# Kernel optimization log

Hardware: AMD Instinct MI355X
Metric: run time of the kernel (lower is better)

## Reference

```python
import jax, jax.numpy as jnp
import numpy as np

E, TOPK, H, I = 8, 2, 2048, 5632
T = 4096


def setup_inputs() -> dict:
    key = jax.random.key(0)
    k1, k2, k3, k4 = jax.random.split(key, 4)
    hidden_states = jax.random.normal(k1, (T, H), dtype=jnp.float32)
    gate_w = jax.random.normal(k2, (E, H), dtype=jnp.float32) * (1.0 / np.sqrt(H))
    # fused gate+up projection: [E, 2*I, H]
    w13 = jax.random.normal(k3, (E, 2 * I, H), dtype=jnp.float32) * (1.0 / np.sqrt(H))
    # down projection: [E, H, I]
    w2 = jax.random.normal(k4, (E, H, I), dtype=jnp.float32) * (1.0 / np.sqrt(I))
    return {"hidden_states": hidden_states, "gate_w": gate_w, "w13": w13, "w2": w2, "top_k": TOPK}


def reference(hidden_states, gate_w, w13, w2, top_k):
    num_experts = gate_w.shape[0]
    inter = w2.shape[2]
    # router: fp32 gate logits -> softmax -> top-k -> renormalize (FusedMoE renormalize=True)
    logits = hidden_states.astype(jnp.float32) @ gate_w.T          # [T, E]
    probs = jax.nn.softmax(logits, axis=-1)
    vals, idx = jax.lax.top_k(probs, top_k)                        # [T, k]
    vals = vals / jnp.sum(vals, axis=-1, keepdims=True)
    # dense routing weight matrix [T, E] (zero outside top-k)
    dense_w = jnp.sum(jax.nn.one_hot(idx, num_experts, dtype=vals.dtype) * vals[..., None], axis=1)

    def body(acc, inputs):
        w13_e, w2_e, we = inputs                                   # [2I,H], [H,I], [T]
        gu = hidden_states @ w13_e.T                               # [T, 2I]
        g, u = gu[:, :inter], gu[:, inter:]
        h = jax.nn.silu(g) * u                                     # SwiGLU
        y = h @ w2_e.T                                             # [T, H]
        return acc + we[:, None] * y, None

    acc0 = jnp.zeros_like(hidden_states)
    out, _ = jax.lax.scan(body, acc0, (w13, w2, dense_w.T))
    return out
```

## Files before the change

### kernel.cpp

```cpp
#include <hip/hip_runtime.h>

#define T_TOK 4096
#define H_DIM 2048
#define I_DIM 5632
#define NE 8

typedef _Float16 f16;
typedef _Float16 f16x8 __attribute__((ext_vector_type(8)));
typedef _Float16 f16x4 __attribute__((ext_vector_type(4)));
typedef float f32x4 __attribute__((ext_vector_type(4)));

#define OFF_META   0
#define OFF_BTOK   256
#define OFF_BW     (256 + 32768)
#define OFF_RE     (256 + 2 * 32768)
#define OFF_RW     (256 + 3 * 32768)
#define OFF_HSB    (256 + 4 * 32768)
#define OFF_HB     (OFF_HSB + (size_t)T_TOK * H_DIM * 2)

__device__ __forceinline__ int swz(int row, int bir) {
    return (bir & 15) | ((((bir >> 4) ^ row) & 3) << 4);
}

__global__ void cvt_hs_kernel(const float* __restrict__ hs, f16* __restrict__ hsb) {
    size_t i = ((size_t)blockIdx.x * 256 + threadIdx.x) * 8;
    float4 a = *(const float4*)(hs + i);
    float4 b = *(const float4*)(hs + i + 4);
    f16x8 v;
    v[0] = (f16)a.x; v[1] = (f16)a.y; v[2] = (f16)a.z; v[3] = (f16)a.w;
    v[4] = (f16)b.x; v[5] = (f16)b.y; v[6] = (f16)b.z; v[7] = (f16)b.w;
    *(f16x8*)(hsb + i) = v;
}

__global__ void gate_kernel(const float* __restrict__ hs, const float* __restrict__ gw,
                            int* __restrict__ re, float* __restrict__ rw,
                            int* __restrict__ counts) {
    int lane = threadIdx.x & 63;
    int t = blockIdx.x * 4 + (threadIdx.x >> 6);
    float acc[NE];
#pragma unroll
    for (int e = 0; e < NE; ++e) acc[e] = 0.f;
    const float* x = hs + (size_t)t * H_DIM;
    for (int i = lane; i < H_DIM; i += 64) {
        float xv = x[i];
#pragma unroll
        for (int e = 0; e < NE; ++e) acc[e] += xv * gw[e * H_DIM + i];
    }
#pragma unroll
    for (int e = 0; e < NE; ++e)
        for (int off = 32; off > 0; off >>= 1) acc[e] += __shfl_xor(acc[e], off);
    if (lane == 0) {
        int i1 = 0; float l1 = acc[0];
#pragma unroll
        for (int e = 1; e < NE; ++e) if (acc[e] > l1) { l1 = acc[e]; i1 = e; }
        int i2 = -1; float l2 = -1e30f;
#pragma unroll
        for (int e = 0; e < NE; ++e) if (e != i1 && acc[e] > l2) { l2 = acc[e]; i2 = e; }
        float aa = __expf(l2 - l1);
        float s = 1.f / (1.f + aa);
        re[t * 2] = i1; re[t * 2 + 1] = i2;
        rw[t * 2] = s;  rw[t * 2 + 1] = aa * s;
        atomicAdd(&counts[i1], 1);
        atomicAdd(&counts[i2], 1);
    }
}

__global__ void scan_kernel(int* __restrict__ meta) {
    if (threadIdx.x == 0) {
        int s = 0;
        for (int e = 0; e < NE; ++e) { meta[8 + e] = s; meta[16 + e] = s; s += meta[e]; }
    }
}

__global__ void place_kernel(const int* __restrict__ re, const float* __restrict__ rw,
                             int* __restrict__ cursor, int* __restrict__ btok,
                             float* __restrict__ bwv) {
    int t = blockIdx.x * 256 + threadIdx.x;
    if (t >= T_TOK) return;
#pragma unroll
    for (int s = 0; s < 2; ++s) {
        int e = re[t * 2 + s];
        int p = atomicAdd(&cursor[e], 1);
        btok[p] = t;
        bwv[p] = rw[t * 2 + s];
    }
}

__global__ __launch_bounds__(256) void gemm1_kernel(
    const float* __restrict__ w13, const f16* __restrict__ hsb, f16* __restrict__ hb,
    const int* __restrict__ counts, const int* __restrict__ offs,
    const int* __restrict__ btok, int e_arg, int global_h)
{
    const int e = (e_arg >= 0) ? e_arg : (int)blockIdx.z;
    const int n_e = counts[e];
    const int by = blockIdx.y;
    if (by * 128 >= n_e) return;
    const int boff = offs[e];
    const int bx = blockIdx.x;
    const float* We = w13 + (size_t)e * (2 * I_DIM) * H_DIM;

    const int tid = threadIdx.x;
    const int lane = tid & 63;
    const int wid = tid >> 6;
    const int wm = wid >> 1, wn = wid & 1;

    __shared__ f16 As[128 * 32];
    __shared__ f16 Bgs[64 * 32];
    __shared__ f16 Bus[64 * 32];
    char* AsB = (char*)As; char* BgB = (char*)Bgs; char* BuB = (char*)Bus;

    const f16* gA[2];
#pragma unroll
    for (int i = 0; i < 2; ++i) {
        int c = i * 256 + tid;
        int r = c >> 2;
        int idx = by * 128 + r;
        idx = idx < n_e ? idx : (n_e - 1);
        int tok = btok[boff + idx];
        gA[i] = hsb + (size_t)tok * H_DIM + (c & 3) * 8;
    }
    const float* gBg[2]; const float* gBu[2];
#pragma unroll
    for (int j = 0; j < 2; ++j) {
        int lin = j * 256 + tid;
        int r = lin >> 3;
        int k = (lin & 7) * 4;
        gBg[j] = We + (size_t)(bx * 64 + r) * H_DIM + k;
        gBu[j] = We + (size_t)(I_DIM + bx * 64 + r) * H_DIM + k;
    }

    f32x4 accg[4][2], accu[4][2];
#pragma unroll
    for (int m = 0; m < 4; ++m)
#pragma unroll
        for (int n = 0; n < 2; ++n) { accg[m][n] = (f32x4)0.f; accu[m][n] = (f32x4)0.f; }

    const int NT = H_DIM / 32;
    f16x8 av0, av1; float4 bg0, bg1, bu0, bu1;
    av0 = *(const f16x8*)(gA[0]); av1 = *(const f16x8*)(gA[1]);
    bg0 = *(const float4*)(gBg[0]); bg1 = *(const float4*)(gBg[1]);
    bu0 = *(const float4*)(gBu[0]); bu1 = *(const float4*)(gBu[1]);

    for (int kt = 0; kt < NT; ++kt) {
        __syncthreads();
        {
            int c = tid;               int r = c >> 2;
            *(f16x8*)(AsB + r * 64 + swz(r, (c & 3) * 16)) = av0;
            c = 256 + tid;             r = c >> 2;
            *(f16x8*)(AsB + r * 64 + swz(r, (c & 3) * 16)) = av1;
        }
#pragma unroll
        for (int j = 0; j < 2; ++j) {
            int lin = j * 256 + tid; int r = lin >> 3; int bir = (lin & 7) * 8;
            float4 bg = j ? bg1 : bg0;
            float4 bu = j ? bu1 : bu0;
            f16x4 g4, u4;
            g4[0] = (f16)bg.x; g4[1] = (f16)bg.y; g4[2] = (f16)bg.z; g4[3] = (f16)bg.w;
            u4[0] = (f16)bu.x; u4[1] = (f16)bu.y; u4[2] = (f16)bu.z; u4[3] = (f16)bu.w;
            *(f16x4*)(BgB + r * 64 + swz(r, bir)) = g4;
            *(f16x4*)(BuB + r * 64 + swz(r, bir)) = u4;
        }
        __syncthreads();
        if (kt + 1 < NT) {
            int k0 = (kt + 1) * 32;
            av0 = *(const f16x8*)(gA[0] + k0); av1 = *(const f16x8*)(gA[1] + k0);
            bg0 = *(const float4*)(gBg[0] + k0); bg1 = *(const float4*)(gBg[1] + k0);
            bu0 = *(const float4*)(gBu[0] + k0); bu1 = *(const float4*)(gBu[1] + k0);
        }
        f16x8 a[4], bgf[2], buf_[2];
        const int kb = (lane >> 4) * 16;
#pragma unroll
        for (int m = 0; m < 4; ++m) {
            int r = wm * 64 + m * 16 + (lane & 15);
            a[m] = *(const f16x8*)(AsB + r * 64 + swz(r, kb));
        }
#pragma unroll
        for (int n = 0; n < 2; ++n) {
            int r = wn * 32 + n * 16 + (lane & 15);
            bgf[n]  = *(const f16x8*)(BgB + r * 64 + swz(r, kb));
            buf_[n] = *(const f16x8*)(BuB + r * 64 + swz(r, kb));
        }
#pragma unroll
        for (int m = 0; m < 4; ++m)
#pragma unroll
            for (int n = 0; n < 2; ++n) {
                accg[m][n] = __builtin_amdgcn_mfma_f32_16x16x32_f16(a[m], bgf[n],  accg[m][n], 0, 0, 0);
                accu[m][n] = __builtin_amdgcn_mfma_f32_16x16x32_f16(a[m], buf_[n], accu[m][n], 0, 0, 0);
            }
    }
    const int hbase = (global_h ? boff : 0) + by * 128;
#pragma unroll
    for (int m = 0; m < 4; ++m) {
        int rl0 = wm * 64 + m * 16 + ((lane >> 4) << 2);
#pragma unroll
        for (int r = 0; r < 4; ++r) {
            int rl = rl0 + r;
            if (by * 128 + rl < n_e) {
#pragma unroll
                for (int n = 0; n < 2; ++n) {
                    float g = accg[m][n][r];
                    float u = accu[m][n][r];
                    float h = g / (1.f + __expf(-g)) * u;
                    hb[(size_t)(hbase + rl) * I_DIM + bx * 64 + wn * 32 + n * 16 + (lane & 15)] = (f16)h;
                }
            }
        }
    }
}

__global__ __launch_bounds__(256) void gemm2_kernel(
    const float* __restrict__ w2, const f16* __restrict__ hb, float* __restrict__ out,
    const int* __restrict__ counts, const int* __restrict__ offs,
    const int* __restrict__ btok, const float* __restrict__ bwv, int e_arg, int global_h)
{
    const int e = (e_arg >= 0) ? e_arg : (int)blockIdx.z;
    const int n_e = counts[e];
    const int by = blockIdx.y;
    if (by * 128 >= n_e) return;
    const int boff = offs[e];
    const int bx = blockIdx.x;
    const float* We = w2 + (size_t)e * H_DIM * I_DIM;

    const int tid = threadIdx.x;
    const int lane = tid & 63;
    const int wid = tid >> 6;
    const int wm = wid >> 1, wn = wid & 1;

    __shared__ f16 As[128 * 32];
    __shared__ f16 Bs[128 * 32];
    char* AsB = (char*)As; char* BsB = (char*)Bs;

    const int hbase = (global_h ? boff : 0) + by * 128;
    const f16* gA[2];
#pragma unroll
    for (int i = 0; i < 2; ++i) {
        int c = i * 256 + tid;
        int r = c >> 2;
        gA[i] = hb + (size_t)(hbase + r) * I_DIM + (c & 3) * 8;
    }
    const float* gB[4];
#pragma unroll
    for (int j = 0; j < 4; ++j) {
        int lin = j * 256 + tid;
        int r = lin >> 3;
        int k = (lin & 7) * 4;
        gB[j] = We + (size_t)(bx * 128 + r) * I_DIM + k;
    }

    f32x4 acc[4][4];
#pragma unroll
    for (int m = 0; m < 4; ++m)
#pragma unroll
        for (int n = 0; n < 4; ++n) acc[m][n] = (f32x4)0.f;

    const int NT = I_DIM / 32;
    f16x8 av0, av1; float4 bv0, bv1, bv2, bv3;
    av0 = *(const f16x8*)(gA[0]); av1 = *(const f16x8*)(gA[1]);
    bv0 = *(const float4*)(gB[0]); bv1 = *(const float4*)(gB[1]);
    bv2 = *(const float4*)(gB[2]); bv3 = *(const float4*)(gB[3]);

    for (int kt = 0; kt < NT; ++kt) {
        __syncthreads();
        {
            int c = tid;       int r = c >> 2;
            *(f16x8*)(AsB + r * 64 + swz(r, (c & 3) * 16)) = av0;
            c = 256 + tid;     r = c >> 2;
            *(f16x8*)(AsB + r * 64 + swz(r, (c & 3) * 16)) = av1;
        }
#pragma unroll
        for (int j = 0; j < 4; ++j) {
            int lin = j * 256 + tid; int r = lin >> 3; int bir = (lin & 7) * 8;
            float4 b = (j == 0) ? bv0 : (j == 1) ? bv1 : (j == 2) ? bv2 : bv3;
            f16x4 b4;
            b4[0] = (f16)b.x; b4[1] = (f16)b.y; b4[2] = (f16)b.z; b4[3] = (f16)b.w;
            *(f16x4*)(BsB + r * 64 + swz(r, bir)) = b4;
        }
        __syncthreads();
        if (kt + 1 < NT) {
            int k0 = (kt + 1) * 32;
            av0 = *(const f16x8*)(gA[0] + k0); av1 = *(const f16x8*)(gA[1] + k0);
            bv0 = *(const float4*)(gB[0] + k0); bv1 = *(const float4*)(gB[1] + k0);
            bv2 = *(const float4*)(gB[2] + k0); bv3 = *(const float4*)(gB[3] + k0);
        }
        f16x8 a[4], b[4];
        const int kb = (lane >> 4) * 16;
#pragma unroll
        for (int m = 0; m < 4; ++m) {
            int r = wm * 64 + m * 16 + (lane & 15);
            a[m] = *(const f16x8*)(AsB + r * 64 + swz(r, kb));
        }
#pragma unroll
        for (int n = 0; n < 4; ++n) {
            int r = wn * 64 + n * 16 + (lane & 15);
            b[n] = *(const f16x8*)(BsB + r * 64 + swz(r, kb));
        }
#pragma unroll
        for (int m = 0; m < 4; ++m)
#pragma unroll
            for (int n = 0; n < 4; ++n)
                acc[m][n] = __builtin_amdgcn_mfma_f32_16x16x32_f16(a[m], b[n], acc[m][n], 0, 0, 0);
    }
#pragma unroll
    for (int m = 0; m < 4; ++m) {
        int rl0 = wm * 64 + m * 16 + ((lane >> 4) << 2);
#pragma unroll
        for (int r = 0; r < 4; ++r) {
            int rl = rl0 + r;
            if (by * 128 + rl < n_e) {
                int p = boff + by * 128 + rl;
                int tok = btok[p];
                float w = bwv[p];
#pragma unroll
                for (int n = 0; n < 4; ++n) {
                    atomicAdd(&out[(size_t)tok * H_DIM + bx * 128 + wn * 64 + n * 16 + (lane & 15)],
                              w * acc[m][n][r]);
                }
            }
        }
    }
}

extern "C" void kernel_launch(void* const* d_in, const int* in_sizes, int n_in,
                              void* d_out, int out_size, void* d_ws, size_t ws_size,
                              hipStream_t stream) {
    const float* hs  = (const float*)d_in[0];
    const float* gw  = (const float*)d_in[1];
    const float* w13 = (const float*)d_in[2];
    const float* w2  = (const float*)d_in[3];
    float* out = (float*)d_out;

    char* ws = (char*)d_ws;
    int*   meta = (int*)(ws + OFF_META);
    int*   btok = (int*)(ws + OFF_BTOK);
    float* bwv  = (float*)(ws + OFF_BW);
    int*   re   = (int*)(ws + OFF_RE);
    float* rw   = (float*)(ws + OFF_RW);
    f16*   hsb  = (f16*)(ws + OFF_HSB);
    f16*   hb   = (f16*)(ws + OFF_HB);

    hipMemsetAsync(d_out, 0, (size_t)T_TOK * H_DIM * 4, stream);
    hipMemsetAsync(meta, 0, 256, stream);

    cvt_hs_kernel<<<(T_TOK * H_DIM) / (256 * 8), 256, 0, stream>>>(hs, hsb);
    gate_kernel<<<T_TOK / 4, 256, 0, stream>>>(hs, gw, re, rw, meta);
    scan_kernel<<<1, 64, 0, stream>>>(meta);
    place_kernel<<<T_TOK / 256, 256, 0, stream>>>(re, rw, meta + 16, btok, bwv);

    size_t need_allpairs = OFF_HB + (size_t)(2 * T_TOK + 128) * I_DIM * 2;
    if (ws_size >= need_allpairs) {
        gemm1_kernel<<<dim3(I_DIM / 64, T_TOK / 128, NE), 256, 0, stream>>>(
            w13, hsb, hb, meta, meta + 8, btok, -1, 1);
        gemm2_kernel<<<dim3(H_DIM / 128, T_TOK / 128, NE), 256, 0, stream>>>(
            w2, hb, out, meta, meta + 8, btok, bwv, -1, 1);
    } else {
        for (int e = 0; e < NE; ++e) {
            gemm1_kernel<<<dim3(I_DIM / 64, T_TOK / 128, 1), 256, 0, stream>>>(
                w13, hsb, hb, meta, meta + 8, btok, e, 0);
            gemm2_kernel<<<dim3(H_DIM / 128, T_TOK / 128, 1), 256, 0, stream>>>(
                w2, hb, out, meta, meta + 8, btok, bwv, e, 0);
        }
    }
}
```

Measured before the change: 1.405 ms.

## Double-buffer MoE GEMMs with direct global-to-LDS loads, larger tiles, XCD-aware block remap

Both expert GEMMs move to 512-thread blocks with 256-row M tiles and 64-wide K steps. LDS is now double-buffered: activation tiles are loaded with global_load_lds, and weight tiles are converted to fp16 and written into the next buffer while MFMAs run on the current one, synchronised by manual waitcnt and barriers. The grid is flattened to 1D with a remap that spreads logical tiles across the 8 XCDs for better L2 locality. This aims to overlap memory with compute and halve barrier count, at the cost of more LDS per block and fragile hand-written wait counts.

```diff
diff --git a/kernel.cpp b/kernel.cpp
--- a/kernel.cpp
+++ b/kernel.cpp
@@ -18,8 +18,19 @@
 #define OFF_HSB    (256 + 4 * 32768)
 #define OFF_HB     (OFF_HSB + (size_t)T_TOK * H_DIM * 2)
 
-__device__ __forceinline__ int swz(int row, int bir) {
-    return (bir & 15) | ((((bir >> 4) ^ row) & 3) << 4);
+typedef const __attribute__((address_space(1))) unsigned int guint;
+typedef __attribute__((address_space(3))) unsigned int luint;
+
+#define WAITVM4()  asm volatile("s_waitcnt vmcnt(4)" ::: "memory")
+#define WAITVM0()  asm volatile("s_waitcnt vmcnt(0)" ::: "memory")
+#define WAITLG0()  asm volatile("s_waitcnt lgkmcnt(0)" ::: "memory")
+
+__device__ __forceinline__ int swzk(int r, int bir) {
+    return (bir & 15) | ((((bir >> 4) ^ r) & 7) << 4);
+}
+
+__device__ __forceinline__ f16x4 cvt4(float4 v) {
+    f16x4 t; t[0] = (f16)v.x; t[1] = (f16)v.y; t[2] = (f16)v.z; t[3] = (f16)v.w; return t;
 }
 
 __global__ void cvt_hs_kernel(const float* __restrict__ hs, f16* __restrict__ hsb) {
@@ -86,17 +97,24 @@
     }
 }
 
-__global__ __launch_bounds__(256) void gemm1_kernel(
+__global__ __launch_bounds__(512, 2) void gemm1_kernel(
     const float* __restrict__ w13, const f16* __restrict__ hsb, f16* __restrict__ hb,
     const int* __restrict__ counts, const int* __restrict__ offs,
     const int* __restrict__ btok, int e_arg, int global_h)
 {
-    const int e = (e_arg >= 0) ? e_arg : (int)blockIdx.z;
+    const int nwg = gridDim.x;
+    const int cpx = nwg >> 3;
+    const int lin = blockIdx.x;
+    const int logical = (lin & 7) * cpx + (lin >> 3);
+    const int by = logical & 15;
+    const int rest = logical >> 4;
+    int bx, e;
+    if (e_arg >= 0) { bx = rest; e = e_arg; }
+    else            { bx = rest % 88; e = rest / 88; }
+
     const int n_e = counts[e];
-    const int by = blockIdx.y;
-    if (by * 128 >= n_e) return;
+    if (by * 256 >= n_e) return;
     const int boff = offs[e];
-    const int bx = blockIdx.x;
     const float* We = w13 + (size_t)e * (2 * I_DIM) * H_DIM;
 
     const int tid = threadIdx.x;
@@ -104,29 +122,36 @@
     const int wid = tid >> 6;
     const int wm = wid >> 1, wn = wid & 1;
 
-    __shared__ f16 As[128 * 32];
-    __shared__ f16 Bgs[64 * 32];
-    __shared__ f16 Bus[64 * 32];
-    char* AsB = (char*)As; char* BgB = (char*)Bgs; char* BuB = (char*)Bus;
-
-    const f16* gA[2];
-#pragma unroll
-    for (int i = 0; i < 2; ++i) {
-        int c = i * 256 + tid;
-        int r = c >> 2;
-        int idx = by * 128 + r;
-        idx = idx < n_e ? idx : (n_e - 1);
+    __shared__ f16 As[2][256 * 64];
+    __shared__ f16 Bg[2][64 * 64];
+    __shared__ f16 Bu[2][64 * 64];
+    char* AsB = (char*)As;
+    char* BgB = (char*)Bg;
+    char* BuB = (char*)Bu;
+
+    const f16* gA[4];
+    int cgrp[4];
+#pragma unroll
+    for (int i = 0; i < 4; ++i) {
+        int c = wid * 4 + i;
+        cgrp[i] = c;
+        int r = c * 8 + (lane >> 3);
+        int idx = by * 256 + r;
+        idx = idx < n_e ? idx : n_e - 1;
         int tok = btok[boff + idx];
-        gA[i] = hsb + (size_t)tok * H_DIM + (c & 3) * 8;
+        int sg = (lane & 7) ^ (lane >> 3);
+        gA[i] = hsb + (size_t)tok * H_DIM + sg * 8;
     }
     const float* gBg[2]; const float* gBu[2];
+    int bwadr[2];
 #pragma unroll
     for (int j = 0; j < 2; ++j) {
-        int lin = j * 256 + tid;
-        int r = lin >> 3;
-        int k = (lin & 7) * 4;
-        gBg[j] = We + (size_t)(bx * 64 + r) * H_DIM + k;
-        gBu[j] = We + (size_t)(I_DIM + bx * 64 + r) * H_DIM + k;
+        int c = j * 512 + tid;
+        int r = c >> 4;
+        int k4 = c & 15;
+        gBg[j] = We + (size_t)(bx * 64 + r) * H_DIM + k4 * 4;
+        gBu[j] = We + (size_t)(I_DIM + bx * 64 + r) * H_DIM + k4 * 4;
+        bwadr[j] = r * 128 + swzk(r, k4 * 8);
     }
 
     f32x4 accg[4][2], accu[4][2];
@@ -135,67 +160,85 @@
 #pragma unroll
         for (int n = 0; n < 2; ++n) { accg[m][n] = (f32x4)0.f; accu[m][n] = (f32x4)0.f; }
 
-    const int NT = H_DIM / 32;
-    f16x8 av0, av1; float4 bg0, bg1, bu0, bu1;
-    av0 = *(const f16x8*)(gA[0]); av1 = *(const f16x8*)(gA[1]);
-    bg0 = *(const float4*)(gBg[0]); bg1 = *(const float4*)(gBg[1]);
-    bu0 = *(const float4*)(gBu[0]); bu1 = *(const float4*)(gBu[1]);
-
+    const int NT = H_DIM / 64;
+
+    {
+        float4 g0 = *(const float4*)gBg[0];
+        float4 g1 = *(const float4*)gBg[1];
+        float4 u0 = *(const float4*)gBu[0];
+        float4 u1 = *(const float4*)gBu[1];
+        *(f16x4*)(BgB + bwadr[0]) = cvt4(g0);
+        *(f16x4*)(BgB + bwadr[1]) = cvt4(g1);
+        *(f16x4*)(BuB + bwadr[0]) = cvt4(u0);
+        *(f16x4*)(BuB + bwadr[1]) = cvt4(u1);
+#pragma unroll
+        for (int i = 0; i < 4; ++i)
+            __builtin_amdgcn_global_load_lds((guint*)(gA[i]), (luint*)(AsB + cgrp[i] * 1024), 16, 0, 0);
+    }
+
+    int cur = 0;
+#pragma unroll 1
     for (int kt = 0; kt < NT; ++kt) {
-        __syncthreads();
+        const int ktn = (kt + 1 < NT) ? kt + 1 : NT - 1;
+        float4 g0 = *(const float4*)(gBg[0] + ktn * 64);
+        float4 g1 = *(const float4*)(gBg[1] + ktn * 64);
+        float4 u0 = *(const float4*)(gBu[0] + ktn * 64);
+        float4 u1 = *(const float4*)(gBu[1] + ktn * 64);
+        WAITVM4();
+        WAITLG0();
+        __builtin_amdgcn_s_barrier();
+        __builtin_amdgcn_sched_barrier(0);
+#pragma unroll
+        for (int i = 0; i < 4; ++i)
+            __builtin_amdgcn_global_load_lds((guint*)(gA[i] + ktn * 64),
+                (luint*)(AsB + (cur ^ 1) * 32768 + cgrp[i] * 1024), 16, 0, 0);
+        const char* Ab = AsB + cur * 32768;
+        const char* Gb = BgB + cur * 8192;
+        const char* Ub = BuB + cur * 8192;
+#pragma unroll
+        for (int kh = 0; kh < 2; ++kh) {
+            f16x8 a[4], bg[2], bu[2];
+            const int kb = kh * 64 + (lane >> 4) * 16;
+#pragma unroll
+            for (int m = 0; m < 4; ++m) {
+                int r = wm * 64 + m * 16 + (lane & 15);
+                a[m] = *(const f16x8*)(Ab + r * 128 + swzk(r, kb));
+            }
+#pragma unroll
+            for (int n = 0; n < 2; ++n) {
+                int r = wn * 32 + n * 16 + (lane & 15);
+                bg[n] = *(const f16x8*)(Gb + r * 128 + swzk(r, kb));
+                bu[n] = *(const f16x8*)(Ub + r * 128 + swzk(r, kb));
+            }
+#pragma unroll
+            for (int m = 0; m < 4; ++m)
+#pragma unroll
+                for (int n = 0; n < 2; ++n) {
+                    accg[m][n] = __builtin_amdgcn_mfma_f32_16x16x32_f16(a[m], bg[n], accg[m][n], 0, 0, 0);
+                    accu[m][n] = __builtin_amdgcn_mfma_f32_16x16x32_f16(a[m], bu[n], accu[m][n], 0, 0, 0);
+                }
+        }
+        WAITVM4();
         {
-            int c = tid;               int r = c >> 2;
-            *(f16x8*)(AsB + r * 64 + swz(r, (c & 3) * 16)) = av0;
-            c = 256 + tid;             r = c >> 2;
-            *(f16x8*)(AsB + r * 64 + swz(r, (c & 3) * 16)) = av1;
-        }
-#pragma unroll
-        for (int j = 0; j < 2; ++j) {
-            int lin = j * 256 + tid; int r = lin >> 3; int bir = (lin & 7) * 8;
-            float4 bg = j ? bg1 : bg0;
-            float4 bu = j ? bu1 : bu0;
-            f16x4 g4, u4;
-            g4[0] = (f16)bg.x; g4[1] = (f16)bg.y; g4[2] = (f16)bg.z; g4[3] = (f16)bg.w;
-            u4[0] = (f16)bu.x; u4[1] = (f16)bu.y; u4[2] = (f16)bu.z; u4[3] = (f16)bu.w;
-            *(f16x4*)(BgB + r * 64 + swz(r, bir)) = g4;
-            *(f16x4*)(BuB + r * 64 + swz(r, bir)) = u4;
-        }
-        __syncthreads();
-        if (kt + 1 < NT) {
-            int k0 = (kt + 1) * 32;
-            av0 = *(const f16x8*)(gA[0] + k0); av1 = *(const f16x8*)(gA[1] + k0);
-            bg0 = *(const float4*)(gBg[0] + k0); bg1 = *(const float4*)(gBg[1] + k0);
-            bu0 = *(const float4*)(gBu[0] + k0); bu1 = *(const float4*)(gBu[1] + k0);
-        }
-        f16x8 a[4], bgf[2], buf_[2];
-        const int kb = (lane >> 4) * 16;
-#pragma unroll
-        for (int m = 0; m < 4; ++m) {
-            int r = wm * 64 + m * 16 + (lane & 15);
-            a[m] = *(const f16x8*)(AsB + r * 64 + swz(r, kb));
-        }
-#pragma unroll
-        for (int n = 0; n < 2; ++n) {
-            int r = wn * 32 + n * 16 + (lane & 15);
-            bgf[n]  = *(const f16x8*)(BgB + r * 64 + swz(r, kb));
-            buf_[n] = *(const f16x8*)(BuB + r * 64 + swz(r, kb));
-        }
-#pragma unroll
-        for (int m = 0; m < 4; ++m)
-#pragma unroll
-            for (int n = 0; n < 2; ++n) {
-                accg[m][n] = __builtin_amdgcn_mfma_f32_16x16x32_f16(a[m], bgf[n],  accg[m][n], 0, 0, 0);
-                accu[m][n] = __builtin_amdgcn_mfma_f32_16x16x32_f16(a[m], buf_[n], accu[m][n], 0, 0, 0);
-            }
-    }
-    const int hbase = (global_h ? boff : 0) + by * 128;
+            char* Gn = BgB + (cur ^ 1) * 8192;
+            char* Un = BuB + (cur ^ 1) * 8192;
+            *(f16x4*)(Gn + bwadr[0]) = cvt4(g0);
+            *(f16x4*)(Gn + bwadr[1]) = cvt4(g1);
+            *(f16x4*)(Un + bwadr[0]) = cvt4(u0);
+            *(f16x4*)(Un + bwadr[1]) = cvt4(u1);
+        }
+        cur ^= 1;
+    }
+    WAITVM0();
+
+    const int hbase = (global_h ? boff : 0) + by * 256;
 #pragma unroll
     for (int m = 0; m < 4; ++m) {
         int rl0 = wm * 64 + m * 16 + ((lane >> 4) << 2);
 #pragma unroll
         for (int r = 0; r < 4; ++r) {
             int rl = rl0 + r;
-            if (by * 128 + rl < n_e) {
+            if (by * 256 + rl < n_e) {
 #pragma unroll
                 for (int n = 0; n < 2; ++n) {
                     float g = accg[m][n][r];
@@ -208,17 +251,24 @@
     }
 }
 
-__global__ __launch_bounds__(256) void gemm2_kernel(
+__global__ __launch_bounds__(512, 2) void gemm2_kernel(
     const float* __restrict__ w2, const f16* __restrict__ hb, float* __restrict__ out,
     const int* __restrict__ counts, const int* __restrict__ offs,
     const int* __restrict__ btok, const float* __restrict__ bwv, int e_arg, int global_h)
 {
-    const int e = (e_arg >= 0) ? e_arg : (int)blockIdx.z;
+    const int nwg = gridDim.x;
+    const int cpx = nwg >> 3;
+    const int lin = blockIdx.x;
+    const int logical = (lin & 7) * cpx + (lin >> 3);
+    const int by = logical & 15;
+    const int rest = logical >> 4;
+    int bx, e;
+    if (e_arg >= 0) { bx = rest; e = e_arg; }
+    else            { bx = rest % 16; e = rest / 16; }
+
     const int n_e = counts[e];
-    const int by = blockIdx.y;
-    if (by * 128 >= n_e) return;
+    if (by * 256 >= n_e) return;
     const int boff = offs[e];
-    const int bx = blockIdx.x;
     const float* We = w2 + (size_t)e * H_DIM * I_DIM;
 
     const int tid = threadIdx.x;
@@ -226,25 +276,31 @@
     const int wid = tid >> 6;
     const int wm = wid >> 1, wn = wid & 1;
 
-    __shared__ f16 As[128 * 32];
-    __shared__ f16 Bs[128 * 32];
-    char* AsB = (char*)As; char* BsB = (char*)Bs;
-
-    const int hbase = (global_h ? boff : 0) + by * 128;
-    const f16* gA[2];
-#pragma unroll
-    for (int i = 0; i < 2; ++i) {
-        int c = i * 256 + tid;
-        int r = c >> 2;
-        gA[i] = hb + (size_t)(hbase + r) * I_DIM + (c & 3) * 8;
+    __shared__ f16 As[2][256 * 64];
+    __shared__ f16 Bs[2][128 * 64];
+    char* AsB = (char*)As;
+    char* BsB = (char*)Bs;
+
+    const int hbase = (global_h ? boff : 0) + by * 256;
+    const f16* gA[4];
+    int cgrp[4];
+#pragma unroll
+    for (int i = 0; i < 4; ++i) {
+        int c = wid * 4 + i;
+        cgrp[i] = c;
+        int r = c * 8 + (lane >> 3);
+        int sg = (lane & 7) ^ (lane >> 3);
+        gA[i] = hb + (size_t)(hbase + r) * I_DIM + sg * 8;
     }
     const float* gB[4];
+    int bwadr[4];
 #pragma unroll
     for (int j = 0; j < 4; ++j) {
-        int lin = j * 256 + tid;
-        int r = lin >> 3;
-        int k = (lin & 7) * 4;
-        gB[j] = We + (size_t)(bx * 128 + r) * I_DIM + k;
+        int c = j * 512 + tid;
+        int r = c >> 4;
+        int k4 = c & 15;
+        gB[j] = We + (size_t)(bx * 128 + r) * I_DIM + k4 * 4;
+        bwadr[j] = r * 128 + swzk(r, k4 * 8);
     }
 
     f32x4 acc[4][4];
@@ -253,68 +309,86 @@
 #pragma unroll
         for (int n = 0; n < 4; ++n) acc[m][n] = (f32x4)0.f;
 
-    const int NT = I_DIM / 32;
-    f16x8 av0, av1; float4 bv0, bv1, bv2, bv3;
-    av0 = *(const f16x8*)(gA[0]); av1 = *(const f16x8*)(gA[1]);
-    bv0 = *(const float4*)(gB[0]); bv1 = *(const float4*)(gB[1]);
-    bv2 = *(const float4*)(gB[2]); bv3 = *(const float4*)(gB[3]);
-
+    const int NT = I_DIM / 64;
+
+    {
+        float4 b0 = *(const float4*)gB[0];
+        float4 b1 = *(const float4*)gB[1];
+        float4 b2 = *(const float4*)gB[2];
+        float4 b3 = *(const float4*)gB[3];
+        *(f16x4*)(BsB + bwadr[0]) = cvt4(b0);
+        *(f16x4*)(BsB + bwadr[1]) = cvt4(b1);
+        *(f16x4*)(BsB + bwadr[2]) = cvt4(b2);
+        *(f16x4*)(BsB + bwadr[3]) = cvt4(b3);
+#pragma unroll
+        for (int i = 0; i < 4; ++i)
+            __builtin_amdgcn_global_load_lds((guint*)(gA[i]), (luint*)(AsB + cgrp[i] * 1024), 16, 0, 0);
+    }
+
+    int cur = 0;
+#pragma unroll 1
     for (int kt = 0; kt < NT; ++kt) {
-        __syncthreads();
+        const int ktn = (kt + 1 < NT) ? kt + 1 : NT - 1;
+        float4 b0 = *(const float4*)(gB[0] + ktn * 64);
+        float4 b1 = *(const float4*)(gB[1] + ktn * 64);
+        float4 b2 = *(const float4*)(gB[2] + ktn * 64);
+        float4 b3 = *(const float4*)(gB[3] + ktn * 64);
+        WAITVM4();
+        WAITLG0();
+        __builtin_amdgcn_s_barrier();
+        __builtin_amdgcn_sched_barrier(0);
+#pragma unroll
+        for (int i = 0; i < 4; ++i)
+            __builtin_amdgcn_global_load_lds((guint*)(gA[i] + ktn * 64),
+                (luint*)(AsB + (cur ^ 1) * 32768 + cgrp[i] * 1024), 16, 0, 0);
+        const char* Ab = AsB + cur * 32768;
+        const char* Bb = BsB + cur * 16384;
+#pragma unroll
+        for (int kh = 0; kh < 2; ++kh) {
+            f16x8 a[4], b[4];
+            const int kb = kh * 64 + (lane >> 4) * 16;
+#pragma unroll
+            for (int m = 0; m < 4; ++m) {
+                int r = wm * 64 + m * 16 + (lane & 15);
+                a[m] = *(const f16x8*)(Ab + r * 128 + swzk(r, kb));
+            }
+#pragma unroll
+            for (int n = 0; n < 4; ++n) {
+                int r = wn * 64 + n * 16 + (lane & 15);
+                b[n] = *(const f16x8*)(Bb + r * 128 + swzk(r, kb));
+            }
+#pragma unroll
+            for (int m = 0; m < 4; ++m)
+#pragma unroll
+                for (int n = 0; n < 4; ++n)
+                    acc[m][n] = __builtin_amdgcn_mfma_f32_16x16x32_f16(a[m], b[n], acc[m][n], 0, 0, 0);
+        }
+        WAITVM4();
         {
-            int c = tid;       int r = c >> 2;
-            *(f16x8*)(AsB + r * 64 + swz(r, (c & 3) * 16)) = av0;
-            c = 256 + tid;     r = c >> 2;
-            *(f16x8*)(AsB + r * 64 + swz(r, (c & 3) * 16)) = av1;
-        }
-#pragma unroll
-        for (int j = 0; j < 4; ++j) {
-            int lin = j * 256 + tid; int r = lin >> 3; int bir = (lin & 7) * 8;
-            float4 b = (j == 0) ? bv0 : (j == 1) ? bv1 : (j == 2) ? bv2 : bv3;
-            f16x4 b4;
-            b4[0] = (f16)b.x; b4[1] = (f16)b.y; b4[2] = (f16)b.z; b4[3] = (f16)b.w;
-            *(f16x4*)(BsB + r * 64 + swz(r, bir)) = b4;
-        }
-        __syncthreads();
-        if (kt + 1 < NT) {
-            int k0 = (kt + 1) * 32;
-            av0 = *(const f16x8*)(gA[0] + k0); av1 = *(const f16x8*)(gA[1] + k0);
-            bv0 = *(const float4*)(gB[0] + k0); bv1 = *(const float4*)(gB[1] + k0);
-            bv2 = *(const float4*)(gB[2] + k0); bv3 = *(const float4*)(gB[3] + k0);
-        }
-        f16x8 a[4], b[4];
-        const int kb = (lane >> 4) * 16;
-#pragma unroll
-        for (int m = 0; m < 4; ++m) {
-            int r = wm * 64 + m * 16 + (lane & 15);
-            a[m] = *(const f16x8*)(AsB + r * 64 + swz(r, kb));
-        }
-#pragma unroll
-        for (int n = 0; n < 4; ++n) {
-            int r = wn * 64 + n * 16 + (lane & 15);
-            b[n] = *(const f16x8*)(BsB + r * 64 + swz(r, kb));
-        }
-#pragma unroll
-        for (int m = 0; m < 4; ++m)
-#pragma unroll
-            for (int n = 0; n < 4; ++n)
-                acc[m][n] = __builtin_amdgcn_mfma_f32_16x16x32_f16(a[m], b[n], acc[m][n], 0, 0, 0);
-    }
+            char* Bn = BsB + (cur ^ 1) * 16384;
+            *(f16x4*)(Bn + bwadr[0]) = cvt4(b0);
+            *(f16x4*)(Bn + bwadr[1]) = cvt4(b1);
+            *(f16x4*)(Bn + bwadr[2]) = cvt4(b2);
+            *(f16x4*)(Bn + bwadr[3]) = cvt4(b3);
+        }
+        cur ^= 1;
+    }
+    WAITVM0();
+
 #pragma unroll
     for (int m = 0; m < 4; ++m) {
         int rl0 = wm * 64 + m * 16 + ((lane >> 4) << 2);
 #pragma unroll
         for (int r = 0; r < 4; ++r) {
             int rl = rl0 + r;
-            if (by * 128 + rl < n_e) {
-                int p = boff + by * 128 + rl;
+            if (by * 256 + rl < n_e) {
+                int p = boff + by * 256 + rl;
                 int tok = btok[p];
                 float w = bwv[p];
 #pragma unroll
-                for (int n = 0; n < 4; ++n) {
+                for (int n = 0; n < 4; ++n)
                     atomicAdd(&out[(size_t)tok * H_DIM + bx * 128 + wn * 64 + n * 16 + (lane & 15)],
                               w * acc[m][n][r]);
-                }
             }
         }
     }
@@ -346,18 +420,14 @@
     scan_kernel<<<1, 64, 0, stream>>>(meta);
     place_kernel<<<T_TOK / 256, 256, 0, stream>>>(re, rw, meta + 16, btok, bwv);
 
-    size_t need_allpairs = OFF_HB + (size_t)(2 * T_TOK + 128) * I_DIM * 2;
+    size_t need_allpairs = OFF_HB + (size_t)(2 * T_TOK + 256) * I_DIM * 2;
     if (ws_size >= need_allpairs) {
-        gemm1_kernel<<<dim3(I_DIM / 64, T_TOK / 128, NE), 256, 0, stream>>>(
-            w13, hsb, hb, meta, meta + 8, btok, -1, 1);
-        gemm2_kernel<<<dim3(H_DIM / 128, T_TOK / 128, NE), 256, 0, stream>>>(
-            w2, hb, out, meta, meta + 8, btok, bwv, -1, 1);
+        gemm1_kernel<<<16 * 88 * NE, 512, 0, stream>>>(w13, hsb, hb, meta, meta + 8, btok, -1, 1);
+        gemm2_kernel<<<16 * 16 * NE, 512, 0, stream>>>(w2, hb, out, meta, meta + 8, btok, bwv, -1, 1);
     } else {
         for (int e = 0; e < NE; ++e) {
-            gemm1_kernel<<<dim3(I_DIM / 64, T_TOK / 128, 1), 256, 0, stream>>>(
-                w13, hsb, hb, meta, meta + 8, btok, e, 0);
-            gemm2_kernel<<<dim3(H_DIM / 128, T_TOK / 128, 1), 256, 0, stream>>>(
-                w2, hb, out, meta, meta + 8, btok, bwv, e, 0);
-        }
-    }
-}
+            gemm1_kernel<<<16 * 88, 512, 0, stream>>>(w13, hsb, hb, meta, meta + 8, btok, e, 0);
+            gemm2_kernel<<<16 * 16, 512, 0, stream>>>(w2, hb, out, meta, meta + 8, btok, bwv, e, 0);
+        }
+    }
+}
```

New measurement: 2.934 ms. 2.09x slower.

## Double K-tile depth and remap blocks to panel-grouped 1D grid for weight reuse

Applied to the files above, without the earlier changes.

Both expert GEMMs now stage 64-wide K tiles instead of 32, halving the number of barrier pairs per tile and doubling the loads in flight, with an 8-way XOR swizzle for the wider shared rows. The 3D grid becomes a 1D grid decoded so that groups of 8 consecutive weight panels sweep all token row-blocks together. Consecutive blocks therefore share the same weight panels in L2, cutting re-reads of the large fp32 weights. The cost is more shared memory and registers per block, which may lower occupancy.

```diff
diff --git a/kernel.cpp b/kernel.cpp
--- a/kernel.cpp
+++ b/kernel.cpp
@@ -18,8 +18,12 @@
 #define OFF_HSB    (256 + 4 * 32768)
 #define OFF_HB     (OFF_HSB + (size_t)T_TOK * H_DIM * 2)
 
-__device__ __forceinline__ int swz(int row, int bir) {
-    return (bir & 15) | ((((bir >> 4) ^ row) & 3) << 4);
+__device__ __forceinline__ int swzk(int r, int bir) {
+    return (bir & 15) | ((((bir >> 4) ^ r) & 7) << 4);
+}
+
+__device__ __forceinline__ f16x4 cvt4(float4 v) {
+    f16x4 t; t[0] = (f16)v.x; t[1] = (f16)v.y; t[2] = (f16)v.z; t[3] = (f16)v.w; return t;
 }
 
 __global__ void cvt_hs_kernel(const float* __restrict__ hs, f16* __restrict__ hsb) {
@@ -86,17 +90,26 @@
     }
 }
 
+__device__ __forceinline__ void decode_panel(int id, int npx, int e_arg,
+                                             int& e, int& bx, int& by) {
+    int sg  = id >> 8;
+    int rem = id & 255;
+    by = rem >> 3;
+    int P = sg * 8 + (rem & 7);
+    if (e_arg >= 0) { e = e_arg; bx = P; }
+    else            { e = P / npx; bx = P % npx; }
+}
+
 __global__ __launch_bounds__(256) void gemm1_kernel(
     const float* __restrict__ w13, const f16* __restrict__ hsb, f16* __restrict__ hb,
     const int* __restrict__ counts, const int* __restrict__ offs,
     const int* __restrict__ btok, int e_arg, int global_h)
 {
-    const int e = (e_arg >= 0) ? e_arg : (int)blockIdx.z;
+    int e, bx, by;
+    decode_panel(blockIdx.x, 88, e_arg, e, bx, by);
     const int n_e = counts[e];
-    const int by = blockIdx.y;
     if (by * 128 >= n_e) return;
     const int boff = offs[e];
-    const int bx = blockIdx.x;
     const float* We = w13 + (size_t)e * (2 * I_DIM) * H_DIM;
 
     const int tid = threadIdx.x;
@@ -104,29 +117,34 @@
     const int wid = tid >> 6;
     const int wm = wid >> 1, wn = wid & 1;
 
-    __shared__ f16 As[128 * 32];
-    __shared__ f16 Bgs[64 * 32];
-    __shared__ f16 Bus[64 * 32];
-    char* AsB = (char*)As; char* BgB = (char*)Bgs; char* BuB = (char*)Bus;
-
-    const f16* gA[2];
-#pragma unroll
-    for (int i = 0; i < 2; ++i) {
+    __shared__ f16 As[128 * 64];
+    __shared__ f16 Bg[64 * 64];
+    __shared__ f16 Bu[64 * 64];
+    char* AsB = (char*)As; char* BgB = (char*)Bg; char* BuB = (char*)Bu;
+
+    const f16* gA[4];
+    int awadr[4];
+#pragma unroll
+    for (int i = 0; i < 4; ++i) {
         int c = i * 256 + tid;
-        int r = c >> 2;
+        int r = c >> 3;
+        int s = c & 7;
         int idx = by * 128 + r;
-        idx = idx < n_e ? idx : (n_e - 1);
+        idx = idx < n_e ? idx : n_e - 1;
         int tok = btok[boff + idx];
-        gA[i] = hsb + (size_t)tok * H_DIM + (c & 3) * 8;
-    }
-    const float* gBg[2]; const float* gBu[2];
-#pragma unroll
-    for (int j = 0; j < 2; ++j) {
-        int lin = j * 256 + tid;
-        int r = lin >> 3;
-        int k = (lin & 7) * 4;
-        gBg[j] = We + (size_t)(bx * 64 + r) * H_DIM + k;
-        gBu[j] = We + (size_t)(I_DIM + bx * 64 + r) * H_DIM + k;
+        gA[i] = hsb + (size_t)tok * H_DIM + s * 8;
+        awadr[i] = r * 128 + swzk(r, s * 16);
+    }
+    const float* gBg[4]; const float* gBu[4];
+    int bwadr[4];
+#pragma unroll
+    for (int j = 0; j < 4; ++j) {
+        int c = j * 256 + tid;
+        int r = c >> 4;
+        int k4 = c & 15;
+        gBg[j] = We + (size_t)(bx * 64 + r) * H_DIM + k4 * 4;
+        gBu[j] = We + (size_t)(I_DIM + bx * 64 + r) * H_DIM + k4 * 4;
+        bwadr[j] = r * 128 + swzk(r, k4 * 8);
     }
 
     f32x4 accg[4][2], accu[4][2];
@@ -135,59 +153,60 @@
 #pragma unroll
         for (int n = 0; n < 2; ++n) { accg[m][n] = (f32x4)0.f; accu[m][n] = (f32x4)0.f; }
 
-    const int NT = H_DIM / 32;
-    f16x8 av0, av1; float4 bg0, bg1, bu0, bu1;
-    av0 = *(const f16x8*)(gA[0]); av1 = *(const f16x8*)(gA[1]);
-    bg0 = *(const float4*)(gBg[0]); bg1 = *(const float4*)(gBg[1]);
-    bu0 = *(const float4*)(gBu[0]); bu1 = *(const float4*)(gBu[1]);
-
+    const int NT = H_DIM / 64;
+
+    f16x8 aR[4]; float4 gR[4], uR[4];
+#pragma unroll
+    for (int i = 0; i < 4; ++i) {
+        aR[i] = *(const f16x8*)(gA[i]);
+        gR[i] = *(const float4*)(gBg[i]);
+        uR[i] = *(const float4*)(gBu[i]);
+    }
+
+#pragma unroll 1
     for (int kt = 0; kt < NT; ++kt) {
         __syncthreads();
-        {
-            int c = tid;               int r = c >> 2;
-            *(f16x8*)(AsB + r * 64 + swz(r, (c & 3) * 16)) = av0;
-            c = 256 + tid;             r = c >> 2;
-            *(f16x8*)(AsB + r * 64 + swz(r, (c & 3) * 16)) = av1;
-        }
-#pragma unroll
-        for (int j = 0; j < 2; ++j) {
-            int lin = j * 256 + tid; int r = lin >> 3; int bir = (lin & 7) * 8;
-            float4 bg = j ? bg1 : bg0;
-            float4 bu = j ? bu1 : bu0;
-            f16x4 g4, u4;
-            g4[0] = (f16)bg.x; g4[1] = (f16)bg.y; g4[2] = (f16)bg.z; g4[3] = (f16)bg.w;
-            u4[0] = (f16)bu.x; u4[1] = (f16)bu.y; u4[2] = (f16)bu.z; u4[3] = (f16)bu.w;
-            *(f16x4*)(BgB + r * 64 + swz(r, bir)) = g4;
-            *(f16x4*)(BuB + r * 64 + swz(r, bir)) = u4;
+#pragma unroll
+        for (int i = 0; i < 4; ++i) {
+            *(f16x8*)(AsB + awadr[i]) = aR[i];
+            *(f16x4*)(BgB + bwadr[i]) = cvt4(gR[i]);
+            *(f16x4*)(BuB + bwadr[i]) = cvt4(uR[i]);
         }
         __syncthreads();
         if (kt + 1 < NT) {
-            int k0 = (kt + 1) * 32;
-            av0 = *(const f16x8*)(gA[0] + k0); av1 = *(const f16x8*)(gA[1] + k0);
-            bg0 = *(const float4*)(gBg[0] + k0); bg1 = *(const float4*)(gBg[1] + k0);
-            bu0 = *(const float4*)(gBu[0] + k0); bu1 = *(const float4*)(gBu[1] + k0);
-        }
-        f16x8 a[4], bgf[2], buf_[2];
-        const int kb = (lane >> 4) * 16;
-#pragma unroll
-        for (int m = 0; m < 4; ++m) {
-            int r = wm * 64 + m * 16 + (lane & 15);
-            a[m] = *(const f16x8*)(AsB + r * 64 + swz(r, kb));
-        }
-#pragma unroll
-        for (int n = 0; n < 2; ++n) {
-            int r = wn * 32 + n * 16 + (lane & 15);
-            bgf[n]  = *(const f16x8*)(BgB + r * 64 + swz(r, kb));
-            buf_[n] = *(const f16x8*)(BuB + r * 64 + swz(r, kb));
-        }
-#pragma unroll
-        for (int m = 0; m < 4; ++m)
+            int k0 = (kt + 1) * 64;
+#pragma unroll
+            for (int i = 0; i < 4; ++i) {
+                aR[i] = *(const f16x8*)(gA[i] + k0);
+                gR[i] = *(const float4*)(gBg[i] + k0);
+                uR[i] = *(const float4*)(gBu[i] + k0);
+            }
+        }
+#pragma unroll
+        for (int kh = 0; kh < 2; ++kh) {
+            f16x8 a[4], bg[2], bu[2];
+            const int kb = kh * 64 + (lane >> 4) * 16;
+#pragma unroll
+            for (int m = 0; m < 4; ++m) {
+                int r = wm * 64 + m * 16 + (lane & 15);
+                a[m] = *(const f16x8*)(AsB + r * 128 + swzk(r, kb));
+            }
 #pragma unroll
             for (int n = 0; n < 2; ++n) {
-                accg[m][n] = __builtin_amdgcn_mfma_f32_16x16x32_f16(a[m], bgf[n],  accg[m][n], 0, 0, 0);
-                accu[m][n] = __builtin_amdgcn_mfma_f32_16x16x32_f16(a[m], buf_[n], accu[m][n], 0, 0, 0);
-            }
-    }
+                int r = wn * 32 + n * 16 + (lane & 15);
+                bg[n] = *(const f16x8*)(BgB + r * 128 + swzk(r, kb));
+                bu[n] = *(const f16x8*)(BuB + r * 128 + swzk(r, kb));
+            }
+#pragma unroll
+            for (int m = 0; m < 4; ++m)
+#pragma unroll
+                for (int n = 0; n < 2; ++n) {
+                    accg[m][n] = __builtin_amdgcn_mfma_f32_16x16x32_f16(a[m], bg[n], accg[m][n], 0, 0, 0);
+                    accu[m][n] = __builtin_amdgcn_mfma_f32_16x16x32_f16(a[m], bu[n], accu[m][n], 0, 0, 0);
+                }
+        }
+    }
+
     const int hbase = (global_h ? boff : 0) + by * 128;
 #pragma unroll
     for (int m = 0; m < 4; ++m) {
@@ -213,12 +232,11 @@
     const int* __restrict__ counts, const int* __restrict__ offs,
     const int* __restrict__ btok, const float* __restrict__ bwv, int e_arg, int global_h)
 {
-    const int e = (e_arg >= 0) ? e_arg : (int)blockIdx.z;
+    int e, bx, by;
+    decode_panel(blockIdx.x, 16, e_arg, e, bx, by);
     const int n_e = counts[e];
-    const int by = blockIdx.y;
     if (by * 128 >= n_e) return;
     const int boff = offs[e];
-    const int bx = blockIdx.x;
     const float* We = w2 + (size_t)e * H_DIM * I_DIM;
 
     const int tid = threadIdx.x;
@@ -226,25 +244,30 @@
     const int wid = tid >> 6;
     const int wm = wid >> 1, wn = wid & 1;
 
-    __shared__ f16 As[128 * 32];
-    __shared__ f16 Bs[128 * 32];
+    __shared__ f16 As[128 * 64];
+    __shared__ f16 Bs[128 * 64];
     char* AsB = (char*)As; char* BsB = (char*)Bs;
 
     const int hbase = (global_h ? boff : 0) + by * 128;
-    const f16* gA[2];
-#pragma unroll
-    for (int i = 0; i < 2; ++i) {
+    const f16* gA[4];
+    int awadr[4];
+#pragma unroll
+    for (int i = 0; i < 4; ++i) {
         int c = i * 256 + tid;
-        int r = c >> 2;
-        gA[i] = hb + (size_t)(hbase + r) * I_DIM + (c & 3) * 8;
-    }
-    const float* gB[4];
-#pragma unroll
-    for (int j = 0; j < 4; ++j) {
-        int lin = j * 256 + tid;
-        int r = lin >> 3;
-        int k = (lin & 7) * 4;
-        gB[j] = We + (size_t)(bx * 128 + r) * I_DIM + k;
+        int r = c >> 3;
+        int s = c & 7;
+        gA[i] = hb + (size_t)(hbase + r) * I_DIM + s * 8;
+        awadr[i] = r * 128 + swzk(r, s * 16);
+    }
+    const float* gB[8];
+    int bwadr[8];
+#pragma unroll
+    for (int j = 0; j < 8; ++j) {
+        int c = j * 256 + tid;
+        int r = c >> 4;
+        int k4 = c & 15;
+        gB[j] = We + (size_t)(bx * 128 + r) * I_DIM + k4 * 4;
+        bwadr[j] = r * 128 + swzk(r, k4 * 8);
     }
 
     f32x4 acc[4][4];
@@ -253,53 +276,51 @@
 #pragma unroll
         for (int n = 0; n < 4; ++n) acc[m][n] = (f32x4)0.f;
 
-    const int NT = I_DIM / 32;
-    f16x8 av0, av1; float4 bv0, bv1, bv2, bv3;
-    av0 = *(const f16x8*)(gA[0]); av1 = *(const f16x8*)(gA[1]);
-    bv0 = *(const float4*)(gB[0]); bv1 = *(const float4*)(gB[1]);
-    bv2 = *(const float4*)(gB[2]); bv3 = *(const float4*)(gB[3]);
-
+    const int NT = I_DIM / 64;
+
+    f16x8 aR[4]; float4 bR[8];
+#pragma unroll
+    for (int i = 0; i < 4; ++i) aR[i] = *(const f16x8*)(gA[i]);
+#pragma unroll
+    for (int j = 0; j < 8; ++j) bR[j] = *(const float4*)(gB[j]);
+
+#pragma unroll 1
     for (int kt = 0; kt < NT; ++kt) {
         __syncthreads();
-        {
-            int c = tid;       int r = c >> 2;
-            *(f16x8*)(AsB + r * 64 + swz(r, (c & 3) * 16)) = av0;
-            c = 256 + tid;     r = c >> 2;
-            *(f16x8*)(AsB + r * 64 + swz(r, (c & 3) * 16)) = av1;
-        }
-#pragma unroll
-        for (int j = 0; j < 4; ++j) {
-            int lin = j * 256 + tid; int r = lin >> 3; int bir = (lin & 7) * 8;
-            float4 b = (j == 0) ? bv0 : (j == 1) ? bv1 : (j == 2) ? bv2 : bv3;
-            f16x4 b4;
-            b4[0] = (f16)b.x; b4[1] = (f16)b.y; b4[2] = (f16)b.z; b4[3] = (f16)b.w;
-            *(f16x4*)(BsB + r * 64 + swz(r, bir)) = b4;
-        }
+#pragma unroll
+        for (int i = 0; i < 4; ++i) *(f16x8*)(AsB + awadr[i]) = aR[i];
+#pragma unroll
+        for (int j = 0; j < 8; ++j) *(f16x4*)(BsB + bwadr[j]) = cvt4(bR[j]);
         __syncthreads();
         if (kt + 1 < NT) {
-            int k0 = (kt + 1) * 32;
-            av0 = *(const f16x8*)(gA[0] + k0); av1 = *(const f16x8*)(gA[1] + k0);
-            bv0 = *(const float4*)(gB[0] + k0); bv1 = *(const float4*)(gB[1] + k0);
-            bv2 = *(const float4*)(gB[2] + k0); bv3 = *(const float4*)(gB[3] + k0);
-        }
-        f16x8 a[4], b[4];
-        const int kb = (lane >> 4) * 16;
-#pragma unroll
-        for (int m = 0; m < 4; ++m) {
-            int r = wm * 64 + m * 16 + (lane & 15);
-            a[m] = *(const f16x8*)(AsB + r * 64 + swz(r, kb));
-        }
-#pragma unroll
-        for (int n = 0; n < 4; ++n) {
-            int r = wn * 64 + n * 16 + (lane & 15);
-            b[n] = *(const f16x8*)(BsB + r * 64 + swz(r, kb));
-        }
-#pragma unroll
-        for (int m = 0; m < 4; ++m)
-#pragma unroll
-            for (int n = 0; n < 4; ++n)
-                acc[m][n] = __builtin_amdgcn_mfma_f32_16x16x32_f16(a[m], b[n], acc[m][n], 0, 0, 0);
-    }
+            int k0 = (kt + 1) * 64;
+#pragma unroll
+            for (int i = 0; i < 4; ++i) aR[i] = *(const f16x8*)(gA[i] + k0);
+#pragma unroll
+            for (int j = 0; j < 8; ++j) bR[j] = *(const float4*)(gB[j] + k0);
+        }
+#pragma unroll
+        for (int kh = 0; kh < 2; ++kh) {
+            f16x8 a[4], b[4];
+            const int kb = kh * 64 + (lane >> 4) * 16;
+#pragma unroll
+            for (int m = 0; m < 4; ++m) {
+                int r = wm * 64 + m * 16 + (lane & 15);
+                a[m] = *(const f16x8*)(AsB + r * 128 + swzk(r, kb));
+            }
+#pragma unroll
+            for (int n = 0; n < 4; ++n) {
+                int r = wn * 64 + n * 16 + (lane & 15);
+                b[n] = *(const f16x8*)(BsB + r * 128 + swzk(r, kb));
+            }
+#pragma unroll
+            for (int m = 0; m < 4; ++m)
+#pragma unroll
+                for (int n = 0; n < 4; ++n)
+                    acc[m][n] = __builtin_amdgcn_mfma_f32_16x16x32_f16(a[m], b[n], acc[m][n], 0, 0, 0);
+        }
+    }
+
 #pragma unroll
     for (int m = 0; m < 4; ++m) {
         int rl0 = wm * 64 + m * 16 + ((lane >> 4) << 2);
@@ -311,10 +332,9 @@
                 int tok = btok[p];
                 float w = bwv[p];
 #pragma unroll
-                for (int n = 0; n < 4; ++n) {
+                for (int n = 0; n < 4; ++n)
                     atomicAdd(&out[(size_t)tok * H_DIM + bx * 128 + wn * 64 + n * 16 + (lane & 15)],
                               w * acc[m][n][r]);
-                }
             }
         }
     }
@@ -348,16 +368,12 @@
 
     size_t need_allpairs = OFF_HB + (size_t)(2 * T_TOK + 128) * I_DIM * 2;
     if (ws_size >= need_allpairs) {
-        gemm1_kernel<<<dim3(I_DIM / 64, T_TOK / 128, NE), 256, 0, stream>>>(
-            w13, hsb, hb, meta, meta + 8, btok, -1, 1);
-        gemm2_kernel<<<dim3(H_DIM / 128, T_TOK / 128, NE), 256, 0, stream>>>(
-            w2, hb, out, meta, meta + 8, btok, bwv, -1, 1);
+        gemm1_kernel<<<704 * 32, 256, 0, stream>>>(w13, hsb, hb, meta, meta + 8, btok, -1, 1);
+        gemm2_kernel<<<128 * 32, 256, 0, stream>>>(w2, hb, out, meta, meta + 8, btok, bwv, -1, 1);
     } else {
         for (int e = 0; e < NE; ++e) {
-            gemm1_kernel<<<dim3(I_DIM / 64, T_TOK / 128, 1), 256, 0, stream>>>(
-                w13, hsb, hb, meta, meta + 8, btok, e, 0);
-            gemm2_kernel<<<dim3(H_DIM / 128, T_TOK / 128, 1), 256, 0, stream>>>(
-                w2, hb, out, meta, meta + 8, btok, bwv, e, 0);
-        }
-    }
-}
+            gemm1_kernel<<<88 * 32, 256, 0, stream>>>(w13, hsb, hb, meta, meta + 8, btok, e, 0);
+            gemm2_kernel<<<16 * 32, 256, 0, stream>>>(w2, hb, out, meta, meta + 8, btok, bwv, e, 0);
+        }
+    }
+}
```

Measured after the change: 1.579 ms. 12.4% more time.
